# Kernel optimization log

Hardware: AMD Instinct MI355X
Metric: run time of the kernel (lower is better)

The kernel has to match this reference:

```python
import jax, jax.numpy as jnp
import numpy as np

B, S, D = 2, 2048, 512
H, HD = 8, 64  # num_heads, hidden_dim; H*HD == D
FF = 2048
EPS = 1e-5


def layer_norm(x, gamma, beta):
    mu = jnp.mean(x, axis=-1, keepdims=True)
    var = jnp.mean(jnp.square(x - mu), axis=-1, keepdims=True)
    return (x - mu) * jax.lax.rsqrt(var + EPS) * gamma + beta


def setup_inputs() -> dict:
    key = jax.random.key(0)
    ks = jax.random.split(key, 16)
    s = 0.02
    return {
        "Q": jax.random.normal(ks[0], (B, S, D), jnp.float32),
        "K": jax.random.normal(ks[1], (B, S, D), jnp.float32),
        "V": jax.random.normal(ks[2], (B, S, D), jnp.float32),
        "mask": jax.random.randint(ks[3], (B, S, S), 0, 2, jnp.int32),
        "Wq": jax.random.normal(ks[4], (D, H * HD), jnp.float32) * s,
        "Wk": jax.random.normal(ks[5], (D, H * HD), jnp.float32) * s,
        "Wv": jax.random.normal(ks[6], (D, H * HD), jnp.float32) * s,
        "Wo": jax.random.normal(ks[7], (H * HD, D), jnp.float32) * s,
        "bo": jnp.zeros((D,), jnp.float32),
        "gamma": jnp.ones((D,), jnp.float32),
        "beta": jnp.zeros((D,), jnp.float32),
        "W1": jax.random.normal(ks[8], (D, FF), jnp.float32) * s,
        "b1": jnp.zeros((FF,), jnp.float32),
        "W2": jax.random.normal(ks[9], (FF, D), jnp.float32) * s,
        "b2": jnp.zeros((D,), jnp.float32),
    }


def reference(Q, K, V, mask, Wq, Wk, Wv, Wo, bo, gamma, beta, W1, b1, W2, b2):
    # NOTE: original torch code calls Z.masked_fill(...) non-inplace and drops
    # the result, so `mask` has no effect on the math. Sequence=False.
    X = V
    # Faithful (interleaving) reshape: [B, S, H*HD] -> [B*H, S, HD]
    q = (Q @ Wq).reshape(B * H, -1, HD)
    k = (K @ Wk).reshape(B * H, -1, HD)
    v = (V @ Wv).reshape(B * H, -1, HD)
    scale = jnp.sqrt(jnp.float32(D))  # sqrt(input_size[2]), not sqrt(hidden_dim)
    scores = jnp.einsum('bqd,bkd->bqk', q, k) / scale  # [B*H, S, S]
    attn = jax.nn.softmax(scores, axis=2)
    Z = jnp.einsum('bqk,bkd->bqd', attn, v)            # [B*H, S, HD]
    Z = Z.reshape(B, -1, H * HD) @ Wo + bo             # [B, S, D]
    Z = layer_norm(X + Z, gamma, beta)
    ffn = (Z @ W1 + b1) @ W2 + b2                      # no activation in source
    return layer_norm(Z + ffn, gamma, beta)
```

## Files before the change

kernel.cpp:

```cpp
#include <hip/hip_runtime.h>
#include <hip/hip_bf16.h>


typedef __hip_bfloat16 bf16;
typedef short s16x8 __attribute__((ext_vector_type(8)));
typedef short s16x4 __attribute__((ext_vector_type(4)));
typedef float f32x4 __attribute__((ext_vector_type(4)));

#if __has_builtin(__builtin_amdgcn_exp2f)
#define EXP2F(x) __builtin_amdgcn_exp2f(x)
#else
#define EXP2F(x) exp2f(x)
#endif

__device__ __forceinline__ int dtypeF32(const void* gamma) {
    return *(const unsigned int*)gamma == 0x3F800000u;
}
__device__ __forceinline__ float inElem(const void* p, size_t i, int f32) {
    return f32 ? ((const float*)p)[i]
               : __bfloat162float(((const bf16*)p)[i]);
}
__device__ __forceinline__ void outElem(void* p, size_t i, float v, int f32) {
    if (f32) ((float*)p)[i] = v;
    else     ((bf16*)p)[i] = __float2bfloat16(v);
}
__device__ __forceinline__ s16x8 load8bf(const void* p, size_t i, int f32) {
    if (f32) {
        const float* s = (const float*)p + i;
        const float4 a = *(const float4*)s;
        const float4 b = *(const float4*)(s + 4);
        bf16 t[8] = {__float2bfloat16(a.x), __float2bfloat16(a.y),
                     __float2bfloat16(a.z), __float2bfloat16(a.w),
                     __float2bfloat16(b.x), __float2bfloat16(b.y),
                     __float2bfloat16(b.z), __float2bfloat16(b.w)};
        return *(const s16x8*)t;
    }
    return *(const s16x8*)((const bf16*)p + i);
}
__device__ __forceinline__ void load8f(const void* p, size_t i, int f32, float* o) {
    if (f32) {
        const float* s = (const float*)p + i;
        const float4 a = *(const float4*)s;
        const float4 b = *(const float4*)(s + 4);
        o[0] = a.x; o[1] = a.y; o[2] = a.z; o[3] = a.w;
        o[4] = b.x; o[5] = b.y; o[6] = b.z; o[7] = b.w;
    } else {
        const s16x8 v = *(const s16x8*)((const bf16*)p + i);
#pragma unroll
        for (int j = 0; j < 8; ++j) o[j] = __bfloat162float(((const bf16*)&v)[j]);
    }
}
__device__ __forceinline__ void store8(void* p, size_t i, const float* v, int f32) {
    if (f32) {
        float4 a = {v[0], v[1], v[2], v[3]};
        float4 b = {v[4], v[5], v[6], v[7]};
        *(float4*)((float*)p + i) = a;
        *(float4*)((float*)p + i + 4) = b;
    } else {
        bf16 t[8];
#pragma unroll
        for (int j = 0; j < 8; ++j) t[j] = __float2bfloat16(v[j]);
        *(s16x8*)((bf16*)p + i) = *(const s16x8*)t;
    }
}

__device__ __forceinline__ void gll16(const bf16* g, unsigned short* l) {
    __builtin_amdgcn_global_load_lds(
        (const __attribute__((address_space(1))) unsigned int*)(const void*)g,
        (__attribute__((address_space(3))) unsigned int*)(void*)l,
        16, 0, 0);
}

__global__ __launch_bounds__(256) void tr_kernel(const void* __restrict__ s0,
                                                 const void* __restrict__ s1,
                                                 const void* __restrict__ s2,
                                                 const void* __restrict__ s3,
                                                 const void* __restrict__ s4,
                                                 bf16* __restrict__ WT4,
                                                 bf16* __restrict__ W2T,
                                                 float scale0,
                                                 const void* __restrict__ gamma) {
    const int z = blockIdx.z;
    if (z < 4 && blockIdx.y >= 16) return;
    const int f32 = dtypeF32(gamma);
    const void* src = z == 0 ? s0 : (z == 1 ? s1 : (z == 2 ? s2 : (z == 3 ? s3 : s4)));
    const int R = (z == 4) ? 2048 : 512;
    const int C = 512;
    bf16* d = (z == 4) ? W2T : WT4 + (size_t)z * 512 * 512;
    const float sc = (z == 0) ? scale0 : 1.f;
    __shared__ bf16 T[32][33];
    const int tx = threadIdx.x & 31, ty = threadIdx.x >> 5;
    const int c0 = blockIdx.x * 32, r0 = blockIdx.y * 32;
#pragma unroll
    for (int i = 0; i < 4; ++i)
        T[ty + 8 * i][tx] = __float2bfloat16(
            sc * inElem(src, (size_t)(r0 + ty + 8 * i) * C + c0 + tx, f32));
    __syncthreads();
#pragma unroll
    for (int i = 0; i < 4; ++i)
        d[(size_t)(c0 + ty + 8 * i) * R + r0 + tx] = T[tx][ty + 8 * i];
}

__global__ __launch_bounds__(256) void proj_kernel(
    const void* __restrict__ Q, const void* __restrict__ K,
    const void* __restrict__ V, const bf16* __restrict__ WT4,
    bf16* __restrict__ Cbase,
    const bf16* __restrict__ W2T, const void* __restrict__ W1,
    float* __restrict__ Wc32, const void* __restrict__ gamma) {
    __shared__ __align__(16) unsigned short smem[20480];

    const int f32 = dtypeF32(gamma);
    const int tid = threadIdx.x;
    const int w = tid >> 6, lane = tid & 63, quad = lane >> 4, l16 = lane & 15;
    const int sr = tid >> 2, sc = (tid & 3) * 8;
    const int blk = blockIdx.x;

    if (blk < 384) {
        typedef unsigned short AsT[64][32];
        typedef unsigned short BsT[256][32];
        AsT* As = (AsT*)smem;
        BsT* Bs = (BsT*)(smem + 4096);

        const int z = blk >> 7, rem = blk & 127, by = rem >> 1, bx = rem & 1;
        const void* A = z == 0 ? Q : (z == 1 ? K : V);
        const bf16* Bt = WT4 + (size_t)z * 512 * 512;
        bf16* C = Cbase + (size_t)z * 4096 * 512;
        const int row0 = by * 64, col0 = bx * 256;

        f32x4 acc[4][4];
#pragma unroll
        for (int rb = 0; rb < 4; ++rb)
#pragma unroll
            for (int nb = 0; nb < 4; ++nb) acc[rb][nb] = (f32x4){0.f, 0.f, 0.f, 0.f};

        const size_t aBase = (size_t)(row0 + sr) * 512 + sc;
        const bf16* gB = Bt + (size_t)(col0 + sr) * 512 + sc;

        {
            const s16x8 a0 = load8bf(A, aBase, f32);
#pragma unroll
            for (int c = 0; c < 4; ++c)
                gll16(gB + (size_t)c * 64 * 512, &Bs[0][c * 64 + sr][sc]);
            *(s16x8*)&As[0][sr][sc] = a0;
        }
        __syncthreads();

        for (int t = 0; t < 16; ++t) {
            const int cur = t & 1, nxt = cur ^ 1;
            s16x8 aN;
            if (t < 15) {
                const int k = (t + 1) * 32;
                aN = load8bf(A, aBase + k, f32);
#pragma unroll
                for (int c = 0; c < 4; ++c)
                    gll16(gB + k + (size_t)c * 64 * 512, &Bs[nxt][c * 64 + sr][sc]);
            }

            s16x8 af[4];
#pragma unroll
            for (int rb = 0; rb < 4; ++rb)
                af[rb] = *(const s16x8*)&As[cur][rb * 16 + l16][quad * 8];
#pragma unroll
            for (int nb = 0; nb < 4; ++nb) {
                const s16x8 bf = *(const s16x8*)&Bs[cur][w * 64 + nb * 16 + l16][quad * 8];
#pragma unroll
                for (int rb = 0; rb < 4; ++rb)
                    acc[rb][nb] = __builtin_amdgcn_mfma_f32_16x16x32_bf16(
                        af[rb], bf, acc[rb][nb], 0, 0, 0);
            }

            if (t < 15) {
                *(s16x8*)&As[nxt][sr][sc] = aN;
                __syncthreads();
            }
        }

#pragma unroll
        for (int rb = 0; rb < 4; ++rb)
#pragma unroll
            for (int nb = 0; nb < 4; ++nb) {
                const int col = col0 + w * 64 + nb * 16 + l16;
#pragma unroll
                for (int r = 0; r < 4; ++r) {
                    const int row = row0 + rb * 16 + quad * 4 + r;
                    C[(size_t)row * 512 + col] = __float2bfloat16(acc[rb][nb][r]);
                }
            }
    } else {
        unsigned short (*As)[40] = (unsigned short (*)[40])smem;
        unsigned short (*Bs)[40] = (unsigned short (*)[40])(smem + 2560);

        const int idx = blk - 384;
        const int bx = idx & 3, by = (idx >> 2) & 7, bz = idx >> 5;
        const int N = 512, Kd = 2048, kSlice = 512;
        const int wr = w >> 1, wc = w & 1;
        const int row0 = by * 64, col0 = bx * 128;
        const int kOff = bz * kSlice;
        float* C = Wc32 + (size_t)bz * N * N;

        f32x4 acc[2][4];
#pragma unroll
        for (int rb = 0; rb < 2; ++rb)
#pragma unroll
            for (int nb = 0; nb < 4; ++nb) acc[rb][nb] = (f32x4){0.f, 0.f, 0.f, 0.f};

        for (int k0 = kOff; k0 < kOff + kSlice; k0 += 32) {
            __syncthreads();
            *(s16x8*)&As[sr][sc] = *(const s16x8*)(W2T + (size_t)(row0 + sr) * Kd + k0 + sc);
            *(s16x8*)&Bs[sr][sc] = load8bf(W1, (size_t)(col0 + sr) * Kd + k0 + sc, f32);
            *(s16x8*)&Bs[sr + 64][sc] = load8bf(W1, (size_t)(col0 + sr + 64) * Kd + k0 + sc, f32);
            __syncthreads();

            s16x8 aF[2], bFr[4];
#pragma unroll
            for (int rb = 0; rb < 2; ++rb)
                aF[rb] = *(const s16x8*)&As[wr * 32 + rb * 16 + l16][quad * 8];
#pragma unroll
            for (int nb = 0; nb < 4; ++nb)
                bFr[nb] = *(const s16x8*)&Bs[wc * 64 + nb * 16 + l16][quad * 8];
#pragma unroll
            for (int rb = 0; rb < 2; ++rb)
#pragma unroll
                for (int nb = 0; nb < 4; ++nb)
                    acc[rb][nb] = __builtin_amdgcn_mfma_f32_16x16x32_bf16(
                        aF[rb], bFr[nb], acc[rb][nb], 0, 0, 0);
        }

#pragma unroll
        for (int rb = 0; rb < 2; ++rb)
#pragma unroll
            for (int nb = 0; nb < 4; ++nb) {
                const int col = col0 + wc * 64 + nb * 16 + l16;
#pragma unroll
                for (int r = 0; r < 4; ++r) {
                    const int row = row0 + wr * 32 + rb * 16 + quad * 4 + r;
                    C[(size_t)row * N + col] = acc[rb][nb][r];
                }
            }
    }
}

__global__ __launch_bounds__(256) void misc_kernel(
    const bf16* __restrict__ Kp, const bf16* __restrict__ Vp,
    bf16* __restrict__ KF, bf16* __restrict__ VF,
    const float* __restrict__ Cf, bf16* __restrict__ WcT,
    const bf16* __restrict__ W2T, const void* __restrict__ b1,
    const void* __restrict__ b2, const void* __restrict__ bo,
    float* __restrict__ bc, float* __restrict__ bo_f,
    const void* __restrict__ gamma) {
    const int b = blockIdx.x, tid = threadIdx.x;
    if (b < 1024) {
        const int fid = b * 256 + tid;
        const int lane = fid & 63, l16 = lane & 15, quad = lane >> 4;
        const int ks = (fid >> 6) & 1;
        const int jb = (fid >> 7) & 127;
        const int g = fid >> 14;
        const bf16* src = Kp + ((size_t)g * 2048 + jb * 16 + l16) * 64 + ks * 32 + quad * 8;
        *(s16x8*)(KF + (size_t)fid * 8) = *(const s16x8*)src;
    } else if (b < 3072) {
        const int fid = (b - 1024) * 256 + tid;
        const int lane = fid & 63, l16 = lane & 15, quad = lane >> 4;
        const int db = (fid >> 6) & 3;
        const int jb = (fid >> 8) & 127;
        const int g = fid >> 15;
        bf16 t[4];
#pragma unroll
        for (int r = 0; r < 4; ++r)
            t[r] = Vp[((size_t)g * 2048 + jb * 16 + quad * 4 + r) * 64 + db * 16 + l16];
        *(s16x4*)(VF + (size_t)fid * 4) = *(const s16x4*)t;
    } else if (b < 3328) {
        const int i = ((b - 3072) * 256 + tid) * 4;
        const int MN = 512 * 512;
        const float4 a = *(const float4*)(Cf + i);
        const float4 b4 = *(const float4*)(Cf + i + MN);
        const float4 c = *(const float4*)(Cf + i + 2 * MN);
        const float4 d = *(const float4*)(Cf + i + 3 * MN);
        bf16 t[4] = {__float2bfloat16(a.x + b4.x + c.x + d.x),
                     __float2bfloat16(a.y + b4.y + c.y + d.y),
                     __float2bfloat16(a.z + b4.z + c.z + d.z),
                     __float2bfloat16(a.w + b4.w + c.w + d.w)};
        *(s16x4*)(WcT + i) = *(const s16x4*)t;
    } else {
        const int f32 = dtypeF32(gamma);
        const int n = (b - 3328) * 4 + (tid >> 6);
        const int lane = tid & 63;
        const bf16* row = W2T + (size_t)n * 2048;
        float s = 0.f;
#pragma unroll
        for (int i = 0; i < 4; ++i) {
            const int f = lane * 8 + 512 * i;
            float b1v[8];
            load8f(b1, f, f32, b1v);
            const s16x8 r = *(const s16x8*)(row + f);
#pragma unroll
            for (int j = 0; j < 8; ++j)
                s += b1v[j] * __bfloat162float(((const bf16*)&r)[j]);
        }
#pragma unroll
        for (int off = 32; off; off >>= 1) s += __shfl_xor(s, off);
        if (lane == 0) {
            bc[n] = s + inElem(b2, n, f32);
            bo_f[n] = inElem(bo, n, f32);
        }
    }
}

__global__ __launch_bounds__(256) void attn_mfma_kernel(const bf16* __restrict__ Qp,
                                                        const bf16* __restrict__ KF,
                                                        const bf16* __restrict__ VF,
                                                        bf16* __restrict__ Z) {
    __shared__ __align__(16) unsigned short KsF[2][8192];
    __shared__ __align__(16) unsigned short VsF[2][8192];

    const int tid = threadIdx.x;
    const int w = tid >> 6;
    const int lane = tid & 63;
    const int quad = lane >> 4;
    const int l16 = lane & 15;

    const int g = blockIdx.x & 15;
    const int qt = blockIdx.x >> 4;
    const int qbase = g * 2048 + qt * 128 + w * 32 + l16;

    s16x8 bQ[2][2];
#pragma unroll
    for (int qf = 0; qf < 2; ++qf)
#pragma unroll
        for (int ks = 0; ks < 2; ++ks)
            bQ[qf][ks] = *(const s16x8*)(Qp + (size_t)(qbase + qf * 16) * 64 + ks * 32 + quad * 8);

    f32x4 o[2][4];
    f32x4 oSum[2];
#pragma unroll
    for (int qf = 0; qf < 2; ++qf) {
        oSum[qf] = (f32x4){0.f, 0.f, 0.f, 0.f};
#pragma unroll
        for (int db = 0; db < 4; ++db) o[qf][db] = (f32x4){0.f, 0.f, 0.f, 0.f};
    }
    const s16x4 aOnes = {(short)0x3F80, (short)0x3F80, (short)0x3F80, (short)0x3F80};

    const bf16* KFg = KF + (size_t)g * 131072;
    const bf16* VFg = VF + (size_t)g * 131072;

#pragma unroll
    for (int c = 0; c < 4; ++c) {
        const int idx = c * 256 + tid;
        gll16(KFg + (size_t)idx * 8, &KsF[0][idx * 8]);
        gll16(VFg + (size_t)idx * 8, &VsF[0][idx * 8]);
    }
    __syncthreads();

    for (int t = 0; t < 16; ++t) {
        const int cur = t & 1, nxt = cur ^ 1;
        if (t < 15) {
            const bf16* kt = KFg + (size_t)(t + 1) * 8192;
            const bf16* vt = VFg + (size_t)(t + 1) * 8192;
#pragma unroll
            for (int c = 0; c < 4; ++c) {
                const int idx = c * 256 + tid;
                gll16(kt + (size_t)idx * 8, &KsF[nxt][idx * 8]);
                gll16(vt + (size_t)idx * 8, &VsF[nxt][idx * 8]);
            }
        }

#pragma unroll
        for (int h = 0; h < 2; ++h) {
            const unsigned short* Kh = &KsF[cur][h * 4096];
            const unsigned short* Vh = &VsF[cur][h * 4096];

            f32x4 st[2][4];
#pragma unroll
            for (int qf = 0; qf < 2; ++qf)
#pragma unroll
                for (int kb = 0; kb < 4; ++kb) st[qf][kb] = (f32x4){0.f, 0.f, 0.f, 0.f};
#pragma unroll
            for (int kb = 0; kb < 4; ++kb)
#pragma unroll
                for (int ks = 0; ks < 2; ++ks) {
                    const s16x8 aK = *(const s16x8*)&Kh[((kb * 2 + ks) * 64 + lane) * 8];
                    st[0][kb] = __builtin_amdgcn_mfma_f32_16x16x32_bf16(aK, bQ[0][ks], st[0][kb], 0, 0, 0);
                    st[1][kb] = __builtin_amdgcn_mfma_f32_16x16x32_bf16(aK, bQ[1][ks], st[1][kb], 0, 0, 0);
                }

            s16x4 bP[2][4];
#pragma unroll
            for (int qf = 0; qf < 2; ++qf)
#pragma unroll
                for (int kb = 0; kb < 4; ++kb) {
                    const float p0 = EXP2F(st[qf][kb][0]);
                    const float p1 = EXP2F(st[qf][kb][1]);
                    const float p2 = EXP2F(st[qf][kb][2]);
                    const float p3 = EXP2F(st[qf][kb][3]);
                    const unsigned lo = __builtin_amdgcn_perm(
                        __builtin_bit_cast(unsigned, p1), __builtin_bit_cast(unsigned, p0), 0x07060302u);
                    const unsigned hi = __builtin_amdgcn_perm(
                        __builtin_bit_cast(unsigned, p3), __builtin_bit_cast(unsigned, p2), 0x07060302u);
                    union { unsigned u[2]; s16x4 v; } cvt;
                    cvt.u[0] = lo; cvt.u[1] = hi;
                    bP[qf][kb] = cvt.v;
                }

#pragma unroll
            for (int kb = 0; kb < 4; ++kb) {
                oSum[0] = __builtin_amdgcn_mfma_f32_16x16x16bf16_1k(aOnes, bP[0][kb], oSum[0], 0, 0, 0);
                oSum[1] = __builtin_amdgcn_mfma_f32_16x16x16bf16_1k(aOnes, bP[1][kb], oSum[1], 0, 0, 0);
#pragma unroll
                for (int db = 0; db < 4; ++db) {
                    const s16x4 aV = *(const s16x4*)&Vh[((kb * 4 + db) * 64 + lane) * 4];
                    o[0][db] = __builtin_amdgcn_mfma_f32_16x16x16bf16_1k(aV, bP[0][kb], o[0][db], 0, 0, 0);
                    o[1][db] = __builtin_amdgcn_mfma_f32_16x16x16bf16_1k(aV, bP[1][kb], o[1][db], 0, 0, 0);
                }
            }
        }

        if (t < 15) __syncthreads();
    }

#pragma unroll
    for (int qf = 0; qf < 2; ++qf) {
        const float inv = 1.f / oSum[qf][0];
        const size_t qrow = (size_t)(qbase + qf * 16);
#pragma unroll
        for (int db = 0; db < 4; ++db) {
            bf16 tmp[4];
#pragma unroll
            for (int r = 0; r < 4; ++r) tmp[r] = __float2bfloat16(o[qf][db][r] * inv);
            *(s16x4*)(Z + qrow * 64 + db * 16 + quad * 4) = *(const s16x4*)tmp;
        }
    }
}

__global__ __launch_bounds__(256) void gemm_bt_kernel(
    const bf16* __restrict__ A, const bf16* __restrict__ Bt,
    const float* __restrict__ bias, bf16* __restrict__ C,
    int M, int N, int K) {
    __shared__ __align__(16) unsigned short As[2][64][32];
    __shared__ __align__(16) unsigned short Bs[2][128][32];

    const int tid = threadIdx.x;
    const int w = tid >> 6, lane = tid & 63, quad = lane >> 4, l16 = lane & 15;
    const int wr = w >> 1, wc = w & 1;
    const int row0 = blockIdx.y * 64, col0 = blockIdx.x * 128;
    const int sr = tid >> 2, sc = (tid & 3) * 8;

    const bf16* gA  = A  + (size_t)(row0 + sr) * K + sc;
    const bf16* gB0 = Bt + (size_t)(col0 + sr) * K + sc;
    const bf16* gB1 = Bt + (size_t)(col0 + sr + 64) * K + sc;

    f32x4 acc[2][4];
#pragma unroll
    for (int rb = 0; rb < 2; ++rb)
#pragma unroll
        for (int nb = 0; nb < 4; ++nb) acc[rb][nb] = (f32x4){0.f, 0.f, 0.f, 0.f};

    const int nst = K >> 5;
    gll16(gA,  &As[0][sr][sc]);
    gll16(gB0, &Bs[0][sr][sc]);
    gll16(gB1, &Bs[0][sr + 64][sc]);
    __syncthreads();

    for (int t = 0; t < nst; ++t) {
        const int cur = t & 1, nxt = cur ^ 1;
        if (t + 1 < nst) {
            const int k = (t + 1) * 32;
            gll16(gA + k,  &As[nxt][sr][sc]);
            gll16(gB0 + k, &Bs[nxt][sr][sc]);
            gll16(gB1 + k, &Bs[nxt][sr + 64][sc]);
        }

        s16x8 aF[2], bF[4];
#pragma unroll
        for (int rb = 0; rb < 2; ++rb)
            aF[rb] = *(const s16x8*)&As[cur][wr * 32 + rb * 16 + l16][quad * 8];
#pragma unroll
        for (int nb = 0; nb < 4; ++nb)
            bF[nb] = *(const s16x8*)&Bs[cur][wc * 64 + nb * 16 + l16][quad * 8];
#pragma unroll
        for (int rb = 0; rb < 2; ++rb)
#pragma unroll
            for (int nb = 0; nb < 4; ++nb)
                acc[rb][nb] = __builtin_amdgcn_mfma_f32_16x16x32_bf16(
                    aF[rb], bF[nb], acc[rb][nb], 0, 0, 0);

        if (t + 1 < nst) __syncthreads();
    }

#pragma unroll
    for (int rb = 0; rb < 2; ++rb)
#pragma unroll
        for (int nb = 0; nb < 4; ++nb) {
            const int col = col0 + wc * 64 + nb * 16 + l16;
            const float bv = bias[col];
#pragma unroll
            for (int r = 0; r < 4; ++r) {
                const int row = row0 + wr * 32 + rb * 16 + quad * 4 + r;
                C[(size_t)row * N + col] = __float2bfloat16(acc[rb][nb][r] + bv);
            }
        }
}

__global__ __launch_bounds__(256) void ln_res_kernel(const void* __restrict__ X, int xMode,
                                                     const bf16* __restrict__ Zin,
                                                     const void* __restrict__ gamma,
                                                     const void* __restrict__ beta,
                                                     void* __restrict__ out, int oMode) {
    const int f = dtypeF32(gamma);
    const int xF = xMode == 2 ? f : xMode;
    const int oF = oMode == 2 ? f : oMode;
    const int row = blockIdx.x * 4 + (threadIdx.x >> 6);
    const int lane = threadIdx.x & 63;
    const size_t rb = (size_t)row * 512;
    const int c0 = lane * 8;

    float v[8];
    load8f(X, rb + c0, xF, v);
    const s16x8 z = *(const s16x8*)(Zin + rb + c0);
    float sum = 0.f, sumsq = 0.f;
#pragma unroll
    for (int i = 0; i < 8; ++i) {
        v[i] += __bfloat162float(((const bf16*)&z)[i]);
        sum += v[i];
        sumsq += v[i] * v[i];
    }
#pragma unroll
    for (int off = 32; off; off >>= 1) {
        sum += __shfl_xor(sum, off);
        sumsq += __shfl_xor(sumsq, off);
    }
    const float mu = sum * (1.f / 512.f);
    const float var = sumsq * (1.f / 512.f) - mu * mu;
    const float rs = rsqrtf(var + 1e-5f);
    float g[8], bt[8], o[8];
    load8f(gamma, c0, f, g);
    load8f(beta, c0, f, bt);
#pragma unroll
    for (int i = 0; i < 8; ++i) o[i] = (v[i] - mu) * rs * g[i] + bt[i];
    store8(out, rb + c0, o, oF);
}

extern "C" void kernel_launch(void* const* d_in, const int* in_sizes, int n_in,
                              void* d_out, int out_size, void* d_ws, size_t ws_size,
                              hipStream_t stream) {
    const void* Q     = d_in[0];
    const void* K     = d_in[1];
    const void* V     = d_in[2];
    const void* Wq    = d_in[4];
    const void* Wk    = d_in[5];
    const void* Wv    = d_in[6];
    const void* Wo    = d_in[7];
    const void* bo    = d_in[8];
    const void* gamma = d_in[9];
    const void* beta  = d_in[10];
    const void* W1    = d_in[11];
    const void* b1    = d_in[12];
    const void* W2    = d_in[13];
    const void* b2    = d_in[14];

    const int M = 4096;
    const size_t NT  = (size_t)M * 512;
    const size_t WSQ = 512 * 512;
    const size_t W1N = 512 * 2048;

    const size_t NEED = 30000000;
    char* scratch = (ws_size >= NEED) ? (char*)d_ws : (char*)d_in[3];

    bf16* base = (bf16*)scratch;
    bf16* Qp  = base;
    bf16* Kp  = Qp + NT;
    bf16* Vp  = Kp + NT;
    bf16* KF  = Vp + NT;
    bf16* VF  = KF + NT;
    bf16* WT4 = VF + NT;
    bf16* W2T = WT4 + 4 * WSQ;
    bf16* WcT = W2T + W1N;
    float* Wc32 = (float*)(WcT + WSQ);
    float* bc   = Wc32 + 4 * WSQ;
    float* bo_f = bc + 512;
    bf16* Zt = Kp;
    bf16* Zo = Qp;
    bf16* Z1 = Vp;
    bf16* Fo = KF;

    const dim3 blk(256);
    const float qscale = 1.4426950408889634f * 0.044194173824159216f;

    tr_kernel<<<dim3(16, 64, 5), blk, 0, stream>>>(Wq, Wk, Wv, Wo, W2,
                                                   WT4, W2T, qscale, gamma);

    proj_kernel<<<dim3(512), blk, 0, stream>>>(Q, K, V, WT4, Qp,
                                               W2T, W1, Wc32, gamma);

    misc_kernel<<<dim3(3456), blk, 0, stream>>>(Kp, Vp, KF, VF, Wc32, WcT,
                                                W2T, b1, b2, bo, bc, bo_f, gamma);

    attn_mfma_kernel<<<dim3(256), blk, 0, stream>>>(Qp, KF, VF, Zt);

    gemm_bt_kernel<<<dim3(4, 64), blk, 0, stream>>>(Zt, WT4 + 3 * WSQ, bo_f,
                                                    Zo, M, 512, 512);
    ln_res_kernel<<<dim3(1024), blk, 0, stream>>>(V, 2, Zo, gamma, beta, Z1, 0);

    gemm_bt_kernel<<<dim3(4, 64), blk, 0, stream>>>(Z1, WcT, bc, Fo, M, 512, 512);
    ln_res_kernel<<<dim3(1024), blk, 0, stream>>>(Z1, 0, Fo, gamma, beta, d_out, 2);
}
```

Baseline: 216.1 us.

## Split attention key range across two wave groups with LDS merge

Doubles the attention block to 512 threads and splits the 16 key tiles between two groups of four waves. Each group streams its own half of K/V through separate double-buffered shared memory. The partial outputs and row sums are then merged through shared memory before normalisation. The aim is more waves per block to hide latency on a 256-block grid, at the cost of double the LDS, an extra merge pass and two more barriers.

```diff
diff --git a/kernel.cpp b/kernel.cpp
--- a/kernel.cpp
+++ b/kernel.cpp
@@ -305,22 +305,26 @@
     }
 }
 
-__global__ __launch_bounds__(256) void attn_mfma_kernel(const bf16* __restrict__ Qp,
+__global__ __launch_bounds__(512) void attn_mfma_kernel(const bf16* __restrict__ Qp,
                                                         const bf16* __restrict__ KF,
                                                         const bf16* __restrict__ VF,
                                                         bf16* __restrict__ Z) {
-    __shared__ __align__(16) unsigned short KsF[2][8192];
-    __shared__ __align__(16) unsigned short VsF[2][8192];
+    __shared__ __align__(16) unsigned short KsF[2][2][8192];
+    __shared__ __align__(16) unsigned short VsF[2][2][8192];
 
     const int tid = threadIdx.x;
     const int w = tid >> 6;
     const int lane = tid & 63;
     const int quad = lane >> 4;
     const int l16 = lane & 15;
+    const int hg = w >> 2;
+    const int wl = w & 3;
+    const int sg = tid >> 8;
+    const int stid = tid & 255;
 
     const int g = blockIdx.x & 15;
     const int qt = blockIdx.x >> 4;
-    const int qbase = g * 2048 + qt * 128 + w * 32 + l16;
+    const int qbase = g * 2048 + qt * 128 + wl * 32 + l16;
 
     s16x8 bQ[2][2];
 #pragma unroll
@@ -341,32 +345,33 @@
 
     const bf16* KFg = KF + (size_t)g * 131072;
     const bf16* VFg = VF + (size_t)g * 131072;
+    const int tb = sg * 8;
 
 #pragma unroll
     for (int c = 0; c < 4; ++c) {
-        const int idx = c * 256 + tid;
-        gll16(KFg + (size_t)idx * 8, &KsF[0][idx * 8]);
-        gll16(VFg + (size_t)idx * 8, &VsF[0][idx * 8]);
+        const int idx = c * 256 + stid;
+        gll16(KFg + (size_t)tb * 8192 + idx * 8, &KsF[sg][0][idx * 8]);
+        gll16(VFg + (size_t)tb * 8192 + idx * 8, &VsF[sg][0][idx * 8]);
     }
     __syncthreads();
 
-    for (int t = 0; t < 16; ++t) {
+    for (int t = 0; t < 8; ++t) {
         const int cur = t & 1, nxt = cur ^ 1;
-        if (t < 15) {
-            const bf16* kt = KFg + (size_t)(t + 1) * 8192;
-            const bf16* vt = VFg + (size_t)(t + 1) * 8192;
+        if (t < 7) {
+            const bf16* kt = KFg + (size_t)(tb + t + 1) * 8192;
+            const bf16* vt = VFg + (size_t)(tb + t + 1) * 8192;
 #pragma unroll
             for (int c = 0; c < 4; ++c) {
-                const int idx = c * 256 + tid;
-                gll16(kt + (size_t)idx * 8, &KsF[nxt][idx * 8]);
-                gll16(vt + (size_t)idx * 8, &VsF[nxt][idx * 8]);
+                const int idx = c * 256 + stid;
+                gll16(kt + (size_t)idx * 8, &KsF[sg][nxt][idx * 8]);
+                gll16(vt + (size_t)idx * 8, &VsF[sg][nxt][idx * 8]);
             }
         }
 
 #pragma unroll
         for (int h = 0; h < 2; ++h) {
-            const unsigned short* Kh = &KsF[cur][h * 4096];
-            const unsigned short* Vh = &VsF[cur][h * 4096];
+            const unsigned short* Kh = &KsF[hg][cur][h * 4096];
+            const unsigned short* Vh = &VsF[hg][cur][h * 4096];
 
             f32x4 st[2][4];
 #pragma unroll
@@ -413,19 +418,40 @@
             }
         }
 
-        if (t < 15) __syncthreads();
-    }
-
-#pragma unroll
-    for (int qf = 0; qf < 2; ++qf) {
-        const float inv = 1.f / oSum[qf][0];
-        const size_t qrow = (size_t)(qbase + qf * 16);
-#pragma unroll
-        for (int db = 0; db < 4; ++db) {
-            bf16 tmp[4];
-#pragma unroll
-            for (int r = 0; r < 4; ++r) tmp[r] = __float2bfloat16(o[qf][db][r] * inv);
-            *(s16x4*)(Z + qrow * 64 + db * 16 + quad * 4) = *(const s16x4*)tmp;
+        if (t < 7) __syncthreads();
+    }
+
+    float* mrg = (float*)&KsF[0][0][0];
+    __syncthreads();
+    if (hg == 1) {
+#pragma unroll
+        for (int qf = 0; qf < 2; ++qf) {
+#pragma unroll
+            for (int db = 0; db < 4; ++db)
+#pragma unroll
+                for (int r = 0; r < 4; ++r)
+                    mrg[((qf * 16 + db * 4 + r) << 8) + wl * 64 + lane] = o[qf][db][r];
+            mrg[((32 + qf) << 8) + wl * 64 + lane] = oSum[qf][0];
+        }
+    }
+    __syncthreads();
+    if (hg == 0) {
+#pragma unroll
+        for (int qf = 0; qf < 2; ++qf) {
+            const float sTot = oSum[qf][0] + mrg[((32 + qf) << 8) + wl * 64 + lane];
+            const float inv = 1.f / sTot;
+            const size_t qrow = (size_t)(qbase + qf * 16);
+#pragma unroll
+            for (int db = 0; db < 4; ++db) {
+                bf16 tmp[4];
+#pragma unroll
+                for (int r = 0; r < 4; ++r) {
+                    const float vv = o[qf][db][r] +
+                        mrg[((qf * 16 + db * 4 + r) << 8) + wl * 64 + lane];
+                    tmp[r] = __float2bfloat16(vv * inv);
+                }
+                *(s16x4*)(Z + qrow * 64 + db * 16 + quad * 4) = *(const s16x4*)tmp;
+            }
         }
     }
 }
@@ -593,7 +619,7 @@
     misc_kernel<<<dim3(3456), blk, 0, stream>>>(Kp, Vp, KF, VF, Wc32, WcT,
                                                 W2T, b1, b2, bo, bc, bo_f, gamma);
 
-    attn_mfma_kernel<<<dim3(256), blk, 0, stream>>>(Qp, KF, VF, Zt);
+    attn_mfma_kernel<<<dim3(256), dim3(512), 0, stream>>>(Qp, KF, VF, Zt);
 
     gemm_bt_kernel<<<dim3(4, 64), blk, 0, stream>>>(Zt, WT4 + 3 * WSQ, bo_f,
                                                     Zo, M, 512, 512);
```

Result: faster. 200.5 us (-7.2%).
